# Kernel optimization log

Measured on AMD Instinct MI355X. Metric: run time of the kernel, lower is better.

Reference implementation:

```python
import jax, jax.numpy as jnp
import numpy as np

N, E, B = 50000, 800000, 64
H, D, FIN = 2, 128, 128  # heads, per-head dim, input feat dim
L = 2  # lstm layers


def segment_softmax(logits, seg, num_segments):
    # logits: [E, ...] softmax over entries sharing seg id (leading axis)
    m = jax.ops.segment_max(logits, seg, num_segments=num_segments)
    e = jnp.exp(logits - m[seg])
    s = jax.ops.segment_sum(e, seg, num_segments=num_segments)
    return e / s[seg]


def gat_layer(x, W, al, ar, b, src, dst):
    # DGL GATConv: fc -> per-edge LeakyReLU score -> edge softmax over dst -> aggregate
    h = (x @ W).reshape(N, H, D)                      # [N,H,D]
    el = jnp.sum(h * al, axis=-1)                     # [N,H]
    er = jnp.sum(h * ar, axis=-1)                     # [N,H]
    e = jax.nn.leaky_relu(el[src] + er[dst], 0.2)     # [E,H]
    alpha = segment_softmax(e, dst, N)                # [E,H]
    out = jax.ops.segment_sum(alpha[:, :, None] * h[src], dst, num_segments=N)
    return out + b                                    # [N,H,D]


def global_attention_pool(x, wg, bg, seg):
    gate = x @ wg + bg                                # [N,1]
    alpha = segment_softmax(gate, seg, B)             # [N,1]
    return jax.ops.segment_sum(alpha * x, seg, num_segments=B)  # [B,F]


def lstm(xs, Wih, Whh, bih, bhh):
    # xs: [T,B,Hd]; params stacked over layers [L,4Hd,Hd]/[L,4Hd]; torch gate order i,f,g,o
    Hd = Whh.shape[-1]
    h = None
    for l in range(Wih.shape[0]):
        def step(carry, x_t, l=l):
            h, c = carry
            gates = x_t @ Wih[l].T + h @ Whh[l].T + bih[l] + bhh[l]
            i, f, g, o = jnp.split(gates, 4, axis=-1)
            c = jax.nn.sigmoid(f) * c + jax.nn.sigmoid(i) * jnp.tanh(g)
            h = jax.nn.sigmoid(o) * jnp.tanh(c)
            return (h, c), h
        init = (jnp.zeros((xs.shape[1], Hd), xs.dtype), jnp.zeros((xs.shape[1], Hd), xs.dtype))
        (h, _), xs = jax.lax.scan(step, init, xs)
    return h  # final hidden state of last layer [B,Hd]


def setup_inputs() -> dict:
    key = jax.random.key(0)
    ks = jax.random.split(key, 32)
    s = 0.1
    inp = {
        "nfeats": jax.random.normal(ks[0], (N, FIN), jnp.float32),
        "src": jax.random.randint(ks[1], (E,), 0, N, jnp.int32),
        "dst": jax.random.randint(ks[2], (E,), 0, N, jnp.int32),
        "node_graph": jnp.sort(jax.random.randint(ks[3], (N,), 0, B, jnp.int32)),
    }
    for i, ink in enumerate([(FIN, ks[4], ks[5], ks[6], ks[7]), (D, ks[8], ks[9], ks[10], ks[11]), (D, ks[12], ks[13], ks[14], ks[15])]):
        fin, kw, kl, kr, kb = ink
        inp[f"W{i+1}"] = jax.random.normal(kw, (fin, H * D), jnp.float32) * s
        inp[f"al{i+1}"] = jax.random.normal(kl, (H, D), jnp.float32) * s
        inp[f"ar{i+1}"] = jax.random.normal(kr, (H, D), jnp.float32) * s
        inp[f"b{i+1}"] = jnp.zeros((H, D), jnp.float32)
    for i in range(4):
        inp[f"gw{i}"] = jax.random.normal(ks[16 + i], (D, 1), jnp.float32) * s
        inp[f"gb{i}"] = jnp.zeros((1,), jnp.float32)
    inp["Wih"] = jax.random.normal(ks[20], (L, 4 * D, D), jnp.float32) * s
    inp["Whh"] = jax.random.normal(ks[21], (L, 4 * D, D), jnp.float32) * s
    inp["bih"] = jnp.zeros((L, 4 * D), jnp.float32)
    inp["bhh"] = jnp.zeros((L, 4 * D), jnp.float32)
    inp["cw"] = jax.random.normal(ks[22], (D, 1), jnp.float32) * s
    inp["cb"] = jnp.zeros((1,), jnp.float32)
    return inp


def reference(nfeats, src, dst, node_graph,
              W1, al1, ar1, b1, W2, al2, ar2, b2, W3, al3, ar3, b3,
              gw0, gb0, gw1, gb1, gw2, gb2, gw3, gb3,
              Wih, Whh, bih, bhh, cw, cb):
    hg0 = global_attention_pool(nfeats, gw0, gb0, node_graph)
    h = jnp.mean(jax.nn.relu(gat_layer(nfeats, W1, al1, ar1, b1, src, dst)), axis=1)
    hg1 = global_attention_pool(h, gw1, gb1, node_graph)
    h = jnp.mean(jax.nn.relu(gat_layer(h, W2, al2, ar2, b2, src, dst)), axis=1)
    hg2 = global_attention_pool(h, gw2, gb2, node_graph)
    h = jnp.mean(jax.nn.relu(gat_layer(h, W3, al3, ar3, b3, src, dst)), axis=1)
    hg3 = global_attention_pool(h, gw3, gb3, node_graph)
    seq = jnp.stack((hg0, hg1, hg2, hg3), axis=0)     # [4,B,D]
    last_h = lstm(seq, Wih, Whh, bih, bhh)            # [B,D] (dropout: eval mode, identity)
    return jax.nn.sigmoid(last_h @ cw + cb)           # [B,1]
```

## Files before the change

kernel.cpp:

```cpp
#include <hip/hip_runtime.h>
#include <cmath>


typedef __attribute__((ext_vector_type(8))) short short8v;
typedef __attribute__((ext_vector_type(4))) float float4v;
typedef __attribute__((ext_vector_type(2))) float float2v;

__device__ __forceinline__ float sigmoidf_(float x){ return 1.f/(1.f+expf(-x)); }
__device__ __forceinline__ float fexp(float x){ return __expf(x); }

__device__ __forceinline__ unsigned f2bf_rne(float f){
  unsigned u = __float_as_uint(f);
  return (u + 0x7fffu + ((u >> 16) & 1u)) >> 16;
}
__device__ __forceinline__ float bf2f(ushort v){ return __uint_as_float((unsigned)v << 16); }
__device__ __forceinline__ unsigned char f2fp8(float f){
  unsigned v = __builtin_amdgcn_cvt_pk_fp8_f32(f, f, 0, false);
  return (unsigned char)(v & 0xffu);
}

__global__ void k_hist(const int* __restrict__ dst, int* __restrict__ deg, int E){
  int e = blockIdx.x*blockDim.x + threadIdx.x;
  if (e < E) atomicAdd(&deg[dst[e]], 1);
}

#define CHUNK 1024
__global__ __launch_bounds__(256) void k_chunksum(const int* __restrict__ in, int* __restrict__ csum, int n){
  int b = blockIdx.x;
  int tid = threadIdx.x;
  int v = 0;
  #pragma unroll
  for (int k = 0; k < 4; k++){
    int i = b*CHUNK + tid + k*256;
    if (i < n) v += in[i];
  }
  for (int d = 1; d < 64; d <<= 1) v += __shfl_xor(v, d);
  __shared__ int ws[4];
  if ((tid & 63) == 0) ws[tid>>6] = v;
  __syncthreads();
  if (tid == 0) csum[b] = ws[0]+ws[1]+ws[2]+ws[3];
}

__global__ __launch_bounds__(256) void k_scan_apply(const int* __restrict__ in, const int* __restrict__ csum,
                                                    int* __restrict__ offs, int n, int nb){
  int b = blockIdx.x;
  int tid = threadIdx.x, lane = tid & 63, wid = tid >> 6;
  __shared__ int s_cpre;
  __shared__ int ws[4];
  if (tid < 64){
    int v = (tid < nb) ? csum[tid] : 0;
    int icl = v;
    for (int d = 1; d < 64; d <<= 1){ int t = __shfl_up(icl, d); if (lane >= d) icl += t; }
    if (tid == b) s_cpre = icl - v;
  }
  __syncthreads();
  int x[4];
  int s = 0;
  #pragma unroll
  for (int k = 0; k < 4; k++){
    int i = b*CHUNK + tid*4 + k;
    x[k] = (i < n) ? in[i] : 0;
    s += x[k];
  }
  int incl = s;
  for (int d = 1; d < 64; d <<= 1){ int t = __shfl_up(incl, d); if (lane >= d) incl += t; }
  if (lane == 63) ws[wid] = incl;
  __syncthreads();
  int wpre = 0;
  for (int w = 0; w < wid; w++) wpre += ws[w];
  int base = s_cpre + wpre + incl - s;
  #pragma unroll
  for (int k = 0; k < 4; k++){
    int i = b*CHUNK + tid*4 + k;
    if (i < n) offs[i] = base;
    base += x[k];
  }
  if (b == nb-1 && tid == 255) offs[n] = base;
}

__global__ void k_scatter_src(const int* __restrict__ src, const int* __restrict__ dst,
                              const int* __restrict__ offs, int* __restrict__ cnt,
                              int* __restrict__ srcP, int E){
  int e = blockIdx.x*blockDim.x + threadIdx.x;
  if (e < E){ int d = dst[e]; int p = atomicAdd(&cnt[d], 1); srcP[offs[d] + p] = src[e]; }
}

__global__ __launch_bounds__(256) void k_prep(
    const int* __restrict__ ng, int* __restrict__ gstart,
    const float* __restrict__ nfeats, const float* __restrict__ gw0, const float* __restrict__ gb0,
    ushort* __restrict__ xh0, float* __restrict__ gate,
    const float* __restrict__ W0, const float* __restrict__ W1, const float* __restrict__ W2,
    ushort* __restrict__ Wt,
    const float* __restrict__ Wih, const float* __restrict__ Whh,
    const float* __restrict__ bih, const float* __restrict__ bhh,
    unsigned* __restrict__ Wxp, unsigned* __restrict__ Whp, float* __restrict__ bias2,
    int N, int B){
  int tid = threadIdx.x;
  int blk = blockIdx.x;
  const int nbGB = (N + 255) >> 8;
  const int nbTG = (N + 3) >> 2;
  const int nbWT = (3*256*128) >> 8;
  if (blk < nbGB){
    int i = blk*256 + tid;
    if (i >= N) return;
    int g = ng[i];
    int gp = (i == 0) ? -1 : ng[i-1];
    for (int bb = gp+1; bb <= g; bb++) gstart[bb] = i;
    if (i == N-1) for (int bb = g+1; bb <= B; bb++) gstart[bb] = N;
    return;
  }
  blk -= nbGB;
  if (blk < nbTG){
    int n = blk*4 + (tid >> 6);
    if (n >= N) return;
    int lane = tid & 63;
    float2 v = *(const float2*)(nfeats + (size_t)n*128 + lane*2);
    unsigned pk = (f2bf_rne(v.y) << 16) | f2bf_rne(v.x);
    *(unsigned*)(xh0 + (size_t)n*128 + lane*2) = pk;
    float2 gv = *(const float2*)(gw0 + lane*2);
    float p = v.x*gv.x + v.y*gv.y;
    for (int k = 1; k < 64; k <<= 1) p += __shfl_xor(p, k);
    if (lane == 0) gate[n] = p + gb0[0];
    return;
  }
  blk -= nbTG;
  if (blk < nbWT){
    int idx = blk*256 + tid;
    int layer = idx >> 15;
    int within = idx & 32767;
    int c = within >> 7;
    int k = within & 127;
    const float* W = (layer == 0) ? W0 : (layer == 1) ? W1 : W2;
    Wt[idx] = (ushort)f2bf_rne(W[(size_t)k*256 + c]);
    return;
  }
  blk -= nbWT;
  {
    int idx = blk*256 + tid;
    if (idx >= 131072) return;
    int j   = idx & 511;
    int c   = (idx >> 9) & 63;
    int isH = (idx >> 15) & 1;
    int l   = idx >> 16;
    const float* srcW = isH ? Whh : Wih;
    float w0 = srcW[(size_t)l*512*128 + (size_t)j*128 + 2*c];
    float w1 = srcW[(size_t)l*512*128 + (size_t)j*128 + 2*c + 1];
    unsigned v = (f2bf_rne(w1) << 16) | f2bf_rne(w0);
    unsigned* dstp = isH ? Whp : Wxp;
    dstp[(size_t)l*32768 + c*512 + j] = v;
    if (!isH && c == 0) bias2[l*512 + j] = bih[l*512 + j] + bhh[l*512 + j];
  }
}

__global__ __launch_bounds__(256) void k_gemm_pool(const ushort* __restrict__ Xh,
    const ushort* __restrict__ Wt, const float* __restrict__ alv, const float* __restrict__ arv,
    unsigned char* __restrict__ Y8, float* __restrict__ el, float* __restrict__ er, int M,
    int gemmBlocks, const float* __restrict__ gate, const int* __restrict__ gstart,
    float* __restrict__ partials){
  __shared__ ushort WlS[16*256*8];
  int tid = threadIdx.x;
  if ((int)blockIdx.x < gemmBlocks){
    #pragma unroll
    for (int i = 0; i < 16; i++){
      int g = i*256 + tid;
      int row = g >> 4, c = g & 15;
      *(uint4*)(WlS + ((size_t)c*256 + row)*8) = *(const uint4*)(Wt + (size_t)row*128 + c*8);
    }
    __syncthreads();
    int wave = tid >> 6;
    int lane = tid & 63;
    int strip = blockIdx.x*4 + wave;
    if (strip*16 >= M) return;
    int m0 = strip*16;
    int l15 = lane & 15;
    int kg  = lane >> 4;
    int arow = m0 + l15; if (arow >= M) arow = M-1;
    short8v a[4];
    const ushort* xrow = Xh + (size_t)arow*128 + kg*8;
    #pragma unroll
    for (int ks = 0; ks < 4; ks++) a[ks] = *(const short8v*)(xrow + ks*32);
    float4v acc[16];
    #pragma unroll
    for (int nt = 0; nt < 16; nt++) acc[nt] = (float4v){0.f,0.f,0.f,0.f};
    #pragma unroll
    for (int nt = 0; nt < 16; nt++){
      #pragma unroll
      for (int ks = 0; ks < 4; ks++){
        short8v b = *(const short8v*)(WlS + (((size_t)(kg + ks*4)*256) + nt*16 + l15)*8);
        acc[nt] = __builtin_amdgcn_mfma_f32_16x16x32_bf16(a[ks], b, acc[nt], 0, 0, 0);
      }
    }
    float pel0[4]={0,0,0,0}, pel1[4]={0,0,0,0}, per0[4]={0,0,0,0}, per1[4]={0,0,0,0};
    #pragma unroll
    for (int nt = 0; nt < 16; nt++){
      int col = nt*16 + l15;
      float av = alv[col], rv = arv[col];
      #pragma unroll
      for (int j = 0; j < 4; j++){
        float v = acc[nt][j];
        int r = m0 + kg*4 + j;
        if (r < M) Y8[(size_t)r*256 + col] = f2fp8(v);
        if (nt < 8){ pel0[j] += v*av; per0[j] += v*rv; }
        else       { pel1[j] += v*av; per1[j] += v*rv; }
      }
    }
    #pragma unroll
    for (int j = 0; j < 4; j++){
      #pragma unroll
      for (int d = 1; d < 16; d <<= 1){
        pel0[j] += __shfl_xor(pel0[j], d);
        pel1[j] += __shfl_xor(pel1[j], d);
        per0[j] += __shfl_xor(per0[j], d);
        per1[j] += __shfl_xor(per1[j], d);
      }
    }
    if (l15 == 0){
      #pragma unroll
      for (int j = 0; j < 4; j++){
        int r = m0 + kg*4 + j;
        if (r < M){
          el[(size_t)r*2+0] = pel0[j];
          el[(size_t)r*2+1] = pel1[j];
          er[(size_t)r*2+0] = per0[j];
          er[(size_t)r*2+1] = per1[j];
        }
      }
    }
  } else {
    float* red = (float*)WlS;
    int pb = blockIdx.x - gemmBlocks;
    int b = pb >> 4;
    int py = pb & 15;
    int lane = tid & 63, wid = tid >> 6;
    int n0 = gstart[b], n1 = gstart[b+1];
    float m = -3.4e38f;
    for (int n = n0 + tid; n < n1; n += 256) m = fmaxf(m, gate[n]);
    for (int k = 1; k < 64; k <<= 1) m = fmaxf(m, __shfl_xor(m, k));
    if (lane == 0) red[wid] = m;
    __syncthreads();
    m = fmaxf(fmaxf(red[0], red[1]), fmaxf(red[2], red[3]));
    __syncthreads();
    float s = 0.f;
    for (int n = n0 + tid; n < n1; n += 256) s += __expf(gate[n] - m);
    for (int k = 1; k < 64; k <<= 1) s += __shfl_xor(s, k);
    if (lane == 0) red[wid] = s;
    __syncthreads();
    s = red[0] + red[1] + red[2] + red[3];
    float inv = (s > 0.f) ? 1.f/s : 0.f;
    int half = tid >> 7, t127 = tid & 127;
    int p = py*2 + half;
    float acc = 0.f;
    for (int n = n0 + p; n < n1; n += 32){
      float w = __expf(gate[n] - m) * inv;
      acc += w * bf2f(Xh[(size_t)n*128 + t127]);
    }
    partials[((size_t)b*32 + p)*128 + t127] = acc;
  }
}

#define MAXE 256
__global__ __launch_bounds__(256) void k_aggregate(const unsigned char* __restrict__ hpair8,
    const float* __restrict__ el, const float* __restrict__ er,
    const int* __restrict__ srcP, const int* __restrict__ offs,
    const float* __restrict__ bias, const float* __restrict__ gwv, const float* __restrict__ gbv,
    ushort* __restrict__ outh, float* __restrict__ gate, int Nn){
  __shared__ float sw[4][MAXE][2];
  __shared__ int   ss[4][MAXE];
  int wave = threadIdx.x >> 6;
  int n = blockIdx.x*4 + wave;
  if (n >= Nn) return;
  int lane = threadIdx.x & 63;
  int e0 = offs[n], e1 = offs[n+1];
  int deg = e1 - e0;
  int quarter = lane >> 4;
  int sub     = lane & 15;
  int head    = sub >> 3;
  float2 erv = *(const float2*)(er + (size_t)n*2);
  float2v acc[8];
  #pragma unroll
  for (int k = 0; k < 8; k++) acc[k] = (float2v){0.f, 0.f};
  float inv0, inv1;

  if (deg <= MAXE){
    float m0 = -3.4e38f, m1 = -3.4e38f;
    for (int i = lane; i < deg; i += 64){
      int s = srcP[e0 + i];
      ss[wave][i] = s;
      float2 lv = *(const float2*)(el + (size_t)s*2);
      float v0 = lv.x + erv.x, v1 = lv.y + erv.y;
      v0 = (v0 > 0.f) ? v0 : 0.2f*v0;
      v1 = (v1 > 0.f) ? v1 : 0.2f*v1;
      sw[wave][i][0] = v0; sw[wave][i][1] = v1;
      m0 = fmaxf(m0, v0); m1 = fmaxf(m1, v1);
    }
    for (int k = 1; k < 64; k <<= 1){ m0 = fmaxf(m0, __shfl_xor(m0, k)); m1 = fmaxf(m1, __shfl_xor(m1, k)); }
    float s0 = 0.f, s1 = 0.f;
    for (int i = lane; i < deg; i += 64){
      float x0 = fexp(sw[wave][i][0] - m0);
      float x1 = fexp(sw[wave][i][1] - m1);
      sw[wave][i][0] = x0; sw[wave][i][1] = x1;
      s0 += x0; s1 += x1;
    }
    for (int k = 1; k < 64; k <<= 1){ s0 += __shfl_xor(s0, k); s1 += __shfl_xor(s1, k); }
    inv0 = (s0 > 0.f) ? 1.f/s0 : 0.f;
    inv1 = (s1 > 0.f) ? 1.f/s1 : 0.f;
    for (int i = quarter; i < deg; i += 4){
      int s = ss[wave][i];
      float w = sw[wave][i][head];
      uint4 hv = *(const uint4*)(hpair8 + (size_t)s*256 + sub*16);
      float2v wv = { w, w };
      acc[0] += wv*__builtin_amdgcn_cvt_pk_f32_fp8(hv.x, false);
      acc[1] += wv*__builtin_amdgcn_cvt_pk_f32_fp8(hv.x, true);
      acc[2] += wv*__builtin_amdgcn_cvt_pk_f32_fp8(hv.y, false);
      acc[3] += wv*__builtin_amdgcn_cvt_pk_f32_fp8(hv.y, true);
      acc[4] += wv*__builtin_amdgcn_cvt_pk_f32_fp8(hv.z, false);
      acc[5] += wv*__builtin_amdgcn_cvt_pk_f32_fp8(hv.z, true);
      acc[6] += wv*__builtin_amdgcn_cvt_pk_f32_fp8(hv.w, false);
      acc[7] += wv*__builtin_amdgcn_cvt_pk_f32_fp8(hv.w, true);
    }
  } else {
    float m0 = -3.4e38f, m1 = -3.4e38f;
    for (int i = e0 + lane; i < e1; i += 64){
      int s = srcP[i];
      float2 lv = *(const float2*)(el + (size_t)s*2);
      float v0 = lv.x + erv.x, v1 = lv.y + erv.y;
      v0 = (v0 > 0.f) ? v0 : 0.2f*v0;
      v1 = (v1 > 0.f) ? v1 : 0.2f*v1;
      m0 = fmaxf(m0, v0); m1 = fmaxf(m1, v1);
    }
    for (int k = 1; k < 64; k <<= 1){ m0 = fmaxf(m0, __shfl_xor(m0, k)); m1 = fmaxf(m1, __shfl_xor(m1, k)); }
    float s0 = 0.f, s1 = 0.f;
    for (int i = e0 + lane; i < e1; i += 64){
      int s = srcP[i];
      float2 lv = *(const float2*)(el + (size_t)s*2);
      float v0 = lv.x + erv.x, v1 = lv.y + erv.y;
      v0 = (v0 > 0.f) ? v0 : 0.2f*v0;
      v1 = (v1 > 0.f) ? v1 : 0.2f*v1;
      s0 += fexp(v0 - m0); s1 += fexp(v1 - m1);
    }
    for (int k = 1; k < 64; k <<= 1){ s0 += __shfl_xor(s0, k); s1 += __shfl_xor(s1, k); }
    inv0 = (s0 > 0.f) ? 1.f/s0 : 0.f;
    inv1 = (s1 > 0.f) ? 1.f/s1 : 0.f;
    for (int c0 = e0; c0 < e1; c0 += 64){
      int ce = e1 - c0; if (ce > 64) ce = 64;
      if (lane < ce){
        int s = srcP[c0 + lane];
        float2 lv = *(const float2*)(el + (size_t)s*2);
        float v0 = lv.x + erv.x, v1 = lv.y + erv.y;
        v0 = (v0 > 0.f) ? v0 : 0.2f*v0;
        v1 = (v1 > 0.f) ? v1 : 0.2f*v1;
        ss[wave][lane] = s;
        sw[wave][lane][0] = fexp(v0 - m0);
        sw[wave][lane][1] = fexp(v1 - m1);
      }
      for (int i = quarter; i < ce; i += 4){
        int s = ss[wave][i];
        float w = sw[wave][i][head];
        uint4 hv = *(const uint4*)(hpair8 + (size_t)s*256 + sub*16);
        float2v wv = { w, w };
        acc[0] += wv*__builtin_amdgcn_cvt_pk_f32_fp8(hv.x, false);
        acc[1] += wv*__builtin_amdgcn_cvt_pk_f32_fp8(hv.x, true);
        acc[2] += wv*__builtin_amdgcn_cvt_pk_f32_fp8(hv.y, false);
        acc[3] += wv*__builtin_amdgcn_cvt_pk_f32_fp8(hv.y, true);
        acc[4] += wv*__builtin_amdgcn_cvt_pk_f32_fp8(hv.z, false);
        acc[5] += wv*__builtin_amdgcn_cvt_pk_f32_fp8(hv.z, true);
        acc[6] += wv*__builtin_amdgcn_cvt_pk_f32_fp8(hv.w, false);
        acc[7] += wv*__builtin_amdgcn_cvt_pk_f32_fp8(hv.w, true);
      }
    }
  }

  float inv = head ? inv1 : inv0;
  #pragma unroll
  for (int k = 0; k < 8; k++){
    float2v t16, t32;
    t16[0] = __shfl_xor(acc[k][0], 16); t16[1] = __shfl_xor(acc[k][1], 16);
    acc[k] += t16;
    t32[0] = __shfl_xor(acc[k][0], 32); t32[1] = __shfl_xor(acc[k][1], 32);
    acc[k] += t32;
  }
  float t[16];
  #pragma unroll
  for (int k = 0; k < 16; k++)
    t[k] = fmaxf(acc[k>>1][k&1]*inv + bias[sub*16 + k], 0.f);
  float o[16];
  #pragma unroll
  for (int k = 0; k < 16; k++) o[k] = 0.5f*(t[k] + __shfl_xor(t[k], 8));
  if (lane < 8){
    ushort u[16];
    #pragma unroll
    for (int k = 0; k < 16; k++) u[k] = (ushort)f2bf_rne(o[k]);
    *(uint4*)(outh + (size_t)n*128 + sub*16)     = *(uint4*)u;
    *(uint4*)(outh + (size_t)n*128 + sub*16 + 8) = *(uint4*)(u + 8);
    float gp = 0.f;
    #pragma unroll
    for (int k = 0; k < 16; k++) gp += o[k]*gwv[sub*16 + k];
    #pragma unroll
    for (int d = 1; d < 8; d <<= 1) gp += __shfl_xor(gp, d);
    if (sub == 0) gate[n] = gp + gbv[0];
  }
}

__global__ __launch_bounds__(512) void k_lstm_all(const float* __restrict__ part4,
    const unsigned* __restrict__ Wxp, const unsigned* __restrict__ Whp,
    const float* __restrict__ bias2,
    const float* __restrict__ cw, const float* __restrict__ cb,
    float* __restrict__ out, int B){
  int b = blockIdx.x;
  int j = threadIdx.x;
  __shared__ float xs[4][128];
  __shared__ float gates[512];
  __shared__ float hcur[128], ccur[128];
  __shared__ float l0out[4][128];
  __shared__ float red[2];

  #pragma unroll
  for (int l = 0; l < 2; l++){
    const unsigned* Wx = Wxp + (size_t)l*32768;
    const unsigned* Wh = Whp + (size_t)l*32768;
    const float* bi = bias2 + l*512;
    { int t = j >> 7, k = j & 127;
      if (l == 0){
        const float* pp = part4 + (((size_t)t*B + b)*32)*128 + k;
        float s = 0.f;
        #pragma unroll
        for (int p2 = 0; p2 < 32; p2++) s += pp[p2*128];
        xs[t][k] = s;
      } else {
        xs[t][k] = l0out[t][k];
      }
      if (j < 128){ hcur[j] = 0.f; ccur[j] = 0.f; } }
    __syncthreads();
    float gx[4] = {0.f, 0.f, 0.f, 0.f};
    #pragma unroll 8
    for (int c = 0; c < 64; c++){
      unsigned w2 = Wx[c*512 + j];
      float wlo = __uint_as_float(w2 << 16);
      float whi = __uint_as_float(w2 & 0xffff0000u);
      #pragma unroll
      for (int t = 0; t < 4; t++)
        gx[t] += xs[t][2*c]*wlo + xs[t][2*c+1]*whi;
    }
    #pragma unroll
    for (int t = 0; t < 4; t++){
      float g = gx[t] + bi[j];
      #pragma unroll 8
      for (int c = 0; c < 64; c++){
        unsigned w2 = Wh[c*512 + j];
        g += hcur[2*c]*__uint_as_float(w2 << 16)
           + hcur[2*c+1]*__uint_as_float(w2 & 0xffff0000u);
      }
      gates[j] = g;
      __syncthreads();
      if (j < 128){
        float gi = sigmoidf_(gates[j]);
        float gf = sigmoidf_(gates[128 + j]);
        float gg = tanhf(gates[256 + j]);
        float go = sigmoidf_(gates[384 + j]);
        float c2 = gf * ccur[j] + gi * gg;
        float h = go * tanhf(c2);
        ccur[j] = c2;
        hcur[j] = h;
        if (l == 0) l0out[t][j] = h;
      }
      __syncthreads();
    }
  }
  float p = (j < 128) ? hcur[j] * cw[j] : 0.f;
  if (j < 128){
    for (int k = 1; k < 64; k <<= 1) p += __shfl_xor(p, k);
    if ((j & 63) == 0) red[j >> 6] = p;
  }
  __syncthreads();
  if (j == 0) out[b] = sigmoidf_(red[0] + red[1] + cb[0]);
}

extern "C" void kernel_launch(void* const* d_in, const int* in_sizes, int n_in,
                              void* d_out, int out_size, void* d_ws, size_t ws_size,
                              hipStream_t stream){
  const float* nfeats = (const float*)d_in[0];
  const int*   src    = (const int*)d_in[1];
  const int*   dst    = (const int*)d_in[2];
  const int*   ng     = (const int*)d_in[3];
  const float* Wm[3]  = { (const float*)d_in[4],  (const float*)d_in[8],  (const float*)d_in[12] };
  const float* al[3]  = { (const float*)d_in[5],  (const float*)d_in[9],  (const float*)d_in[13] };
  const float* ar[3]  = { (const float*)d_in[6],  (const float*)d_in[10], (const float*)d_in[14] };
  const float* bb[3]  = { (const float*)d_in[7],  (const float*)d_in[11], (const float*)d_in[15] };
  const float* gw[4]  = { (const float*)d_in[16], (const float*)d_in[18], (const float*)d_in[20], (const float*)d_in[22] };
  const float* gb[4]  = { (const float*)d_in[17], (const float*)d_in[19], (const float*)d_in[21], (const float*)d_in[23] };
  const float* Wih = (const float*)d_in[24];
  const float* Whh = (const float*)d_in[25];
  const float* bih = (const float*)d_in[26];
  const float* bhh = (const float*)d_in[27];
  const float* cw  = (const float*)d_in[28];
  const float* cb  = (const float*)d_in[29];

  const int N = in_sizes[3];
  const int E = in_sizes[1];
  const int B = out_size;

  char* p = (char*)d_ws;
  auto alloc = [&](size_t bytes) -> void* {
    void* q = (void*)p;
    p += (bytes + 255) & ~(size_t)255;
    return q;
  };
  unsigned char* hpair8 = (unsigned char*)alloc((size_t)N*256);
  ushort* aggh   = (ushort*)alloc((size_t)N*128*2);
  ushort* xh0    = (ushort*)alloc((size_t)N*128*2);
  ushort* Wt     = (ushort*)alloc((size_t)3*256*128*2);
  float*  el     = (float*)alloc((size_t)N*2*4);
  float*  er     = (float*)alloc((size_t)N*2*4);
  int*    srcP   = (int*)alloc((size_t)E*4);
  float*  gate   = (float*)alloc((size_t)N*4);
  int*    deg    = (int*)alloc((size_t)N*4);
  int*    cnt    = (int*)alloc((size_t)N*4);
  int*    offs   = (int*)alloc((size_t)(N+1)*4);
  int*    gstart = (int*)alloc((size_t)(B+1)*4);
  int*    csum   = (int*)alloc((size_t)64*4);
  float*  part4  = (float*)alloc((size_t)4*B*32*128*4);
  unsigned* Wxp  = (unsigned*)alloc((size_t)2*64*512*4);
  unsigned* Whp  = (unsigned*)alloc((size_t)2*64*512*4);
  float*  bias2  = (float*)alloc((size_t)2*512*4);

  auto cdiv = [](int a, int b){ return (a + b - 1) / b; };
  const int NB = cdiv(N, CHUNK);

  hipMemsetAsync(deg, 0, (size_t)((char*)cnt - (char*)deg) + (size_t)N*4, stream);
  k_hist<<<cdiv(E,256), 256, 0, stream>>>(dst, deg, E);
  k_chunksum<<<NB, 256, 0, stream>>>(deg, csum, N);
  k_scan_apply<<<NB, 256, 0, stream>>>(deg, csum, offs, N, NB);
  k_scatter_src<<<cdiv(E,256), 256, 0, stream>>>(src, dst, offs, cnt, srcP, E);

  {
    int nbGB = cdiv(N,256), nbTG = cdiv(N,4), nbWT = (3*256*128)/256, nbLP = cdiv(131072,256);
    k_prep<<<nbGB + nbTG + nbWT + nbLP, 256, 0, stream>>>(
        ng, gstart, nfeats, gw[0], gb[0], xh0, gate,
        Wm[0], Wm[1], Wm[2], Wt, Wih, Whh, bih, bhh, Wxp, Whp, bias2, N, B);
  }

  const int strips = cdiv(N, 16);
  const int gemmBlocks = cdiv(strips, 4);
  const int poolBlocks = B*16;

  const ushort* xh = xh0;
  for (int layer = 0; layer < 3; layer++){
    k_gemm_pool<<<gemmBlocks + poolBlocks, 256, 0, stream>>>(xh, Wt + (size_t)layer*256*128,
        al[layer], ar[layer], hpair8, el, er, N, gemmBlocks, gate, gstart,
        part4 + (size_t)layer*B*32*128);
    k_aggregate<<<cdiv(N,4), 256, 0, stream>>>(hpair8, el, er, srcP, offs,
        bb[layer], gw[layer+1], gb[layer+1], aggh, gate, N);
    xh = aggh;
  }
  k_gemm_pool<<<poolBlocks, 256, 0, stream>>>(aggh, Wt, al[0], ar[0], hpair8, el, er, N,
      0, gate, gstart, part4 + (size_t)3*B*32*128);

  k_lstm_all<<<B, 512, 0, stream>>>(part4, Wxp, Whp, bias2, cw, cb, (float*)d_out, B);
}
```

Before: 433.3 us.

## Move attention-pool blocks from GEMM kernel into aggregate kernel with ping-pong buffers

Splits the combined GEMM+pool launch into a pure MFMA GEMM kernel and folds the global attention pool blocks into the aggregation kernel instead. Double-buffered activation and gate arrays let the pool read the previous layer's features while the aggregation writes the next layer's. The goal is to run the small pool work alongside the long, irregular aggregation rather than the short GEMM, and to slim the GEMM kernel's code. It costs an extra activation and gate buffer, and the pool blocks now share the aggregation kernel's larger shared memory footprint.

```diff
diff --git a/kernel.cpp b/kernel.cpp
--- a/kernel.cpp
+++ b/kernel.cpp
@@ -152,96 +152,106 @@
   }
 }
 
-__global__ __launch_bounds__(256) void k_gemm_pool(const ushort* __restrict__ Xh,
+__global__ __launch_bounds__(256) void k_gemm_mfma(const ushort* __restrict__ Xh,
     const ushort* __restrict__ Wt, const float* __restrict__ alv, const float* __restrict__ arv,
-    unsigned char* __restrict__ Y8, float* __restrict__ el, float* __restrict__ er, int M,
-    int gemmBlocks, const float* __restrict__ gate, const int* __restrict__ gstart,
-    float* __restrict__ partials){
+    unsigned char* __restrict__ Y8, float* __restrict__ el, float* __restrict__ er, int M){
   __shared__ ushort WlS[16*256*8];
   int tid = threadIdx.x;
-  if ((int)blockIdx.x < gemmBlocks){
-    #pragma unroll
-    for (int i = 0; i < 16; i++){
-      int g = i*256 + tid;
-      int row = g >> 4, c = g & 15;
-      *(uint4*)(WlS + ((size_t)c*256 + row)*8) = *(const uint4*)(Wt + (size_t)row*128 + c*8);
-    }
-    __syncthreads();
-    int wave = tid >> 6;
-    int lane = tid & 63;
-    int strip = blockIdx.x*4 + wave;
-    if (strip*16 >= M) return;
-    int m0 = strip*16;
-    int l15 = lane & 15;
-    int kg  = lane >> 4;
-    int arow = m0 + l15; if (arow >= M) arow = M-1;
-    short8v a[4];
-    const ushort* xrow = Xh + (size_t)arow*128 + kg*8;
-    #pragma unroll
-    for (int ks = 0; ks < 4; ks++) a[ks] = *(const short8v*)(xrow + ks*32);
-    float4v acc[16];
-    #pragma unroll
-    for (int nt = 0; nt < 16; nt++) acc[nt] = (float4v){0.f,0.f,0.f,0.f};
-    #pragma unroll
-    for (int nt = 0; nt < 16; nt++){
-      #pragma unroll
-      for (int ks = 0; ks < 4; ks++){
-        short8v b = *(const short8v*)(WlS + (((size_t)(kg + ks*4)*256) + nt*16 + l15)*8);
-        acc[nt] = __builtin_amdgcn_mfma_f32_16x16x32_bf16(a[ks], b, acc[nt], 0, 0, 0);
+  #pragma unroll
+  for (int i = 0; i < 16; i++){
+    int g = i*256 + tid;
+    int row = g >> 4, c = g & 15;
+    *(uint4*)(WlS + ((size_t)c*256 + row)*8) = *(const uint4*)(Wt + (size_t)row*128 + c*8);
+  }
+  __syncthreads();
+  int wave = tid >> 6;
+  int lane = tid & 63;
+  int strip = blockIdx.x*4 + wave;
+  if (strip*16 >= M) return;
+  int m0 = strip*16;
+  int l15 = lane & 15;
+  int kg  = lane >> 4;
+  int arow = m0 + l15; if (arow >= M) arow = M-1;
+  short8v a[4];
+  const ushort* xrow = Xh + (size_t)arow*128 + kg*8;
+  #pragma unroll
+  for (int ks = 0; ks < 4; ks++) a[ks] = *(const short8v*)(xrow + ks*32);
+  float4v acc[16];
+  #pragma unroll
+  for (int nt = 0; nt < 16; nt++) acc[nt] = (float4v){0.f,0.f,0.f,0.f};
+  #pragma unroll
+  for (int nt = 0; nt < 16; nt++){
+    #pragma unroll
+    for (int ks = 0; ks < 4; ks++){
+      short8v b = *(const short8v*)(WlS + (((size_t)(kg + ks*4)*256) + nt*16 + l15)*8);
+      acc[nt] = __builtin_amdgcn_mfma_f32_16x16x32_bf16(a[ks], b, acc[nt], 0, 0, 0);
+    }
+  }
+  float pel0[4]={0,0,0,0}, pel1[4]={0,0,0,0}, per0[4]={0,0,0,0}, per1[4]={0,0,0,0};
+  #pragma unroll
+  for (int nt = 0; nt < 16; nt++){
+    int col = nt*16 + l15;
+    float av = alv[col], rv = arv[col];
+    #pragma unroll
+    for (int j = 0; j < 4; j++){
+      float v = acc[nt][j];
+      int r = m0 + kg*4 + j;
+      if (r < M) Y8[(size_t)r*256 + col] = f2fp8(v);
+      if (nt < 8){ pel0[j] += v*av; per0[j] += v*rv; }
+      else       { pel1[j] += v*av; per1[j] += v*rv; }
+    }
+  }
+  #pragma unroll
+  for (int j = 0; j < 4; j++){
+    #pragma unroll
+    for (int d = 1; d < 16; d <<= 1){
+      pel0[j] += __shfl_xor(pel0[j], d);
+      pel1[j] += __shfl_xor(pel1[j], d);
+      per0[j] += __shfl_xor(per0[j], d);
+      per1[j] += __shfl_xor(per1[j], d);
+    }
+  }
+  if (l15 == 0){
+    #pragma unroll
+    for (int j = 0; j < 4; j++){
+      int r = m0 + kg*4 + j;
+      if (r < M){
+        el[(size_t)r*2+0] = pel0[j];
+        el[(size_t)r*2+1] = pel1[j];
+        er[(size_t)r*2+0] = per0[j];
+        er[(size_t)r*2+1] = per1[j];
       }
     }
-    float pel0[4]={0,0,0,0}, pel1[4]={0,0,0,0}, per0[4]={0,0,0,0}, per1[4]={0,0,0,0};
-    #pragma unroll
-    for (int nt = 0; nt < 16; nt++){
-      int col = nt*16 + l15;
-      float av = alv[col], rv = arv[col];
-      #pragma unroll
-      for (int j = 0; j < 4; j++){
-        float v = acc[nt][j];
-        int r = m0 + kg*4 + j;
-        if (r < M) Y8[(size_t)r*256 + col] = f2fp8(v);
-        if (nt < 8){ pel0[j] += v*av; per0[j] += v*rv; }
-        else       { pel1[j] += v*av; per1[j] += v*rv; }
-      }
-    }
-    #pragma unroll
-    for (int j = 0; j < 4; j++){
-      #pragma unroll
-      for (int d = 1; d < 16; d <<= 1){
-        pel0[j] += __shfl_xor(pel0[j], d);
-        pel1[j] += __shfl_xor(pel1[j], d);
-        per0[j] += __shfl_xor(per0[j], d);
-        per1[j] += __shfl_xor(per1[j], d);
-      }
-    }
-    if (l15 == 0){
-      #pragma unroll
-      for (int j = 0; j < 4; j++){
-        int r = m0 + kg*4 + j;
-        if (r < M){
-          el[(size_t)r*2+0] = pel0[j];
-          el[(size_t)r*2+1] = pel1[j];
-          er[(size_t)r*2+0] = per0[j];
-          er[(size_t)r*2+1] = per1[j];
-        }
-      }
-    }
-  } else {
-    float* red = (float*)WlS;
-    int pb = blockIdx.x - gemmBlocks;
+  }
+}
+
+#define MAXE 256
+__global__ __launch_bounds__(256) void k_agg_pool(const unsigned char* __restrict__ hpair8,
+    const float* __restrict__ el, const float* __restrict__ er,
+    const int* __restrict__ srcP, const int* __restrict__ offs,
+    const float* __restrict__ bias, const float* __restrict__ gwv, const float* __restrict__ gbv,
+    ushort* __restrict__ outh, float* __restrict__ gateOut, int Nn, int nAgg,
+    const ushort* __restrict__ poolX, const float* __restrict__ poolGate,
+    const int* __restrict__ gstart, float* __restrict__ partials){
+  __shared__ float sw[4][MAXE][2];
+  __shared__ int   ss[4][MAXE];
+  int tid = threadIdx.x;
+  if ((int)blockIdx.x >= nAgg){
+    float* red = (float*)sw;
+    int pb = blockIdx.x - nAgg;
     int b = pb >> 4;
     int py = pb & 15;
     int lane = tid & 63, wid = tid >> 6;
     int n0 = gstart[b], n1 = gstart[b+1];
     float m = -3.4e38f;
-    for (int n = n0 + tid; n < n1; n += 256) m = fmaxf(m, gate[n]);
+    for (int n = n0 + tid; n < n1; n += 256) m = fmaxf(m, poolGate[n]);
     for (int k = 1; k < 64; k <<= 1) m = fmaxf(m, __shfl_xor(m, k));
     if (lane == 0) red[wid] = m;
     __syncthreads();
     m = fmaxf(fmaxf(red[0], red[1]), fmaxf(red[2], red[3]));
     __syncthreads();
     float s = 0.f;
-    for (int n = n0 + tid; n < n1; n += 256) s += __expf(gate[n] - m);
+    for (int n = n0 + tid; n < n1; n += 256) s += __expf(poolGate[n] - m);
     for (int k = 1; k < 64; k <<= 1) s += __shfl_xor(s, k);
     if (lane == 0) red[wid] = s;
     __syncthreads();
@@ -251,25 +261,16 @@
     int p = py*2 + half;
     float acc = 0.f;
     for (int n = n0 + p; n < n1; n += 32){
-      float w = __expf(gate[n] - m) * inv;
-      acc += w * bf2f(Xh[(size_t)n*128 + t127]);
+      float w = __expf(poolGate[n] - m) * inv;
+      acc += w * bf2f(poolX[(size_t)n*128 + t127]);
     }
     partials[((size_t)b*32 + p)*128 + t127] = acc;
-  }
-}
-
-#define MAXE 256
-__global__ __launch_bounds__(256) void k_aggregate(const unsigned char* __restrict__ hpair8,
-    const float* __restrict__ el, const float* __restrict__ er,
-    const int* __restrict__ srcP, const int* __restrict__ offs,
-    const float* __restrict__ bias, const float* __restrict__ gwv, const float* __restrict__ gbv,
-    ushort* __restrict__ outh, float* __restrict__ gate, int Nn){
-  __shared__ float sw[4][MAXE][2];
-  __shared__ int   ss[4][MAXE];
-  int wave = threadIdx.x >> 6;
+    return;
+  }
+  int wave = tid >> 6;
   int n = blockIdx.x*4 + wave;
   if (n >= Nn) return;
-  int lane = threadIdx.x & 63;
+  int lane = tid & 63;
   int e0 = offs[n], e1 = offs[n+1];
   int deg = e1 - e0;
   int quarter = lane >> 4;
@@ -397,7 +398,7 @@
     for (int k = 0; k < 16; k++) gp += o[k]*gwv[sub*16 + k];
     #pragma unroll
     for (int d = 1; d < 8; d <<= 1) gp += __shfl_xor(gp, d);
-    if (sub == 0) gate[n] = gp + gbv[0];
+    if (sub == 0) gateOut[n] = gp + gbv[0];
   }
 }
 
@@ -506,13 +507,15 @@
     return q;
   };
   unsigned char* hpair8 = (unsigned char*)alloc((size_t)N*256);
-  ushort* aggh   = (ushort*)alloc((size_t)N*128*2);
+  ushort* agghA  = (ushort*)alloc((size_t)N*128*2);
+  ushort* agghB  = (ushort*)alloc((size_t)N*128*2);
   ushort* xh0    = (ushort*)alloc((size_t)N*128*2);
   ushort* Wt     = (ushort*)alloc((size_t)3*256*128*2);
   float*  el     = (float*)alloc((size_t)N*2*4);
   float*  er     = (float*)alloc((size_t)N*2*4);
   int*    srcP   = (int*)alloc((size_t)E*4);
-  float*  gate   = (float*)alloc((size_t)N*4);
+  float*  gateA  = (float*)alloc((size_t)N*4);
+  float*  gateB  = (float*)alloc((size_t)N*4);
   int*    deg    = (int*)alloc((size_t)N*4);
   int*    cnt    = (int*)alloc((size_t)N*4);
   int*    offs   = (int*)alloc((size_t)(N+1)*4);
@@ -535,25 +538,30 @@
   {
     int nbGB = cdiv(N,256), nbTG = cdiv(N,4), nbWT = (3*256*128)/256, nbLP = cdiv(131072,256);
     k_prep<<<nbGB + nbTG + nbWT + nbLP, 256, 0, stream>>>(
-        ng, gstart, nfeats, gw[0], gb[0], xh0, gate,
+        ng, gstart, nfeats, gw[0], gb[0], xh0, gateA,
         Wm[0], Wm[1], Wm[2], Wt, Wih, Whh, bih, bhh, Wxp, Whp, bias2, N, B);
   }
 
   const int strips = cdiv(N, 16);
   const int gemmBlocks = cdiv(strips, 4);
+  const int aggBlocks  = cdiv(N, 4);
   const int poolBlocks = B*16;
 
-  const ushort* xh = xh0;
+  const ushort* xs[4]  = { xh0, agghA, agghB, agghA };
+  ushort*       xo[3]  = { agghA, agghB, agghA };
+  float*        gs[4]  = { gateA, gateB, gateA, gateB };
+  float*        go[3]  = { gateB, gateA, gateB };
+
   for (int layer = 0; layer < 3; layer++){
-    k_gemm_pool<<<gemmBlocks + poolBlocks, 256, 0, stream>>>(xh, Wt + (size_t)layer*256*128,
-        al[layer], ar[layer], hpair8, el, er, N, gemmBlocks, gate, gstart,
-        part4 + (size_t)layer*B*32*128);
-    k_aggregate<<<cdiv(N,4), 256, 0, stream>>>(hpair8, el, er, srcP, offs,
-        bb[layer], gw[layer+1], gb[layer+1], aggh, gate, N);
-    xh = aggh;
-  }
-  k_gemm_pool<<<poolBlocks, 256, 0, stream>>>(aggh, Wt, al[0], ar[0], hpair8, el, er, N,
-      0, gate, gstart, part4 + (size_t)3*B*32*128);
+    k_gemm_mfma<<<gemmBlocks, 256, 0, stream>>>(xs[layer], Wt + (size_t)layer*256*128,
+        al[layer], ar[layer], hpair8, el, er, N);
+    k_agg_pool<<<aggBlocks + poolBlocks, 256, 0, stream>>>(hpair8, el, er, srcP, offs,
+        bb[layer], gw[layer+1], gb[layer+1], xo[layer], go[layer], N, aggBlocks,
+        xs[layer], gs[layer], gstart, part4 + (size_t)layer*B*32*128);
+  }
+  k_agg_pool<<<poolBlocks, 256, 0, stream>>>(hpair8, el, er, srcP, offs,
+      bb[0], gw[0], gb[0], agghB, gateA, 0, 0,
+      xs[3], gs[3], gstart, part4 + (size_t)3*B*32*128);
 
   k_lstm_all<<<B, 512, 0, stream>>>(part4, Wxp, Whp, bias2, cw, cb, (float*)d_out, B);
 }
```

New measurement: 390.5 us. 1.11x faster.
